# Optimization experiments

Measured on AMD Instinct MI355X. Metric: run time of the kernel, lower is better.

## Reference

```python
import jax, jax.numpy as jnp
import numpy as np

B, F, D, H = 16384, 39, 16, 2   # batch, fields, embed_dim, heads
VOCAB = 10000                    # per-field vocab
DH = D * H                       # attention output dim per layer (no head split)


def setup_inputs() -> dict:
    key = jax.random.key(0)
    ks = jax.random.split(key, 32)
    def n(k, shape, s=0.05):
        return jax.random.normal(k, shape, jnp.float32) * s
    inp = {"x": jax.random.randint(ks[0], (B, F), 0, VOCAB, dtype=jnp.int32)}
    inp["emb"] = n(ks[1], (F * VOCAB, D))
    idx = 2
    for i, din in enumerate([D, DH, DH]):  # layer0: 16->32, layers 1-2: 32->32
        for nm in ["wq", "wk", "wv", "wr"]:
            inp[f"{nm}{i}"] = n(ks[idx], (din, DH)); idx += 1
    prev = F * DH  # 1248 after flatten
    for i, u in enumerate([128, 64, 32, 1], 1):
        inp[f"w{i}"] = n(ks[idx], (prev, u)); idx += 1
        inp[f"b{i}"] = jnp.zeros((u,), jnp.float32)
        prev = u
    return inp


def reference(x, emb,
              wq0, wk0, wv0, wr0,
              wq1, wk1, wv1, wr1,
              wq2, wk2, wv2, wr2,
              w1, b1, w2, b2, w3, b3, w4, b4):
    offsets = jnp.arange(F, dtype=jnp.int32) * VOCAB
    e = emb[x + offsets]                                   # [B, F, D]
    for wq, wk, wv, wr in [(wq0, wk0, wv0, wr0),
                           (wq1, wk1, wv1, wr1),
                           (wq2, wk2, wv2, wr2)]:
        q = jnp.einsum('bfd,de->bfe', e, wq)               # [B, F, DH]
        k = jnp.einsum('bfd,de->bfe', e, wk)
        v = jnp.einsum('bfd,de->bfe', e, wv)
        att = jax.nn.softmax(jnp.einsum('bfe,bge->bfg', q, k), axis=-1)  # [B,F,F], no scaling
        out = jnp.einsum('bfg,bge->bfe', att, v) + jnp.einsum('bfd,de->bfe', e, wr)
        e = jax.nn.relu(out)
    h = e.reshape(B, F * DH)
    for w, b in [(w1, b1), (w2, b2), (w3, b3)]:
        h = jax.nn.relu(h @ w + b)
    return jax.nn.sigmoid(h @ w4 + b4)                     # [B, 1]
```

## Files before the change

### kernel.cpp

```cpp
#include <hip/hip_runtime.h>
#include <math.h>

#define NF   39
#define NB   16384
#define NVOC 10000

typedef unsigned short u16;
typedef unsigned int   u32;
typedef float f32x4 __attribute__((ext_vector_type(4)));
typedef short s16x8 __attribute__((ext_vector_type(8)));

#define E3_U16   20447232u
#define NSWZ     182272

__device__ __forceinline__ u32 bfadj(float x){
    u32 u = __float_as_uint(x);
    return u + 0x7fffu + ((u >> 16) & 1u);
}
__device__ __forceinline__ u32 pk2(float a, float b){
#if __has_builtin(__builtin_amdgcn_cvt_pk_bf16_f32)
    auto t = __builtin_amdgcn_cvt_pk_bf16_f32(a, b);
    u32 r; __builtin_memcpy(&r, &t, 4); return r;
#else
    return __builtin_amdgcn_perm(bfadj(a), bfadj(b), 0x03020706u);
#endif
}
__device__ __forceinline__ u16 f2bf(float f){ return (u16)(bfadj(f) >> 16); }

__device__ __forceinline__ float fexp2(float x){
#if __has_builtin(__builtin_amdgcn_exp2f)
    return __builtin_amdgcn_exp2f(x);
#else
    return exp2f(x);
#endif
}
__device__ __forceinline__ float frcp(float x){
#if __has_builtin(__builtin_amdgcn_rcpf)
    return __builtin_amdgcn_rcpf(x);
#else
    return 1.f / x;
#endif
}

__device__ __forceinline__ void wave_sync(){
    asm volatile("s_waitcnt lgkmcnt(0)" ::: "memory");
}
__device__ __forceinline__ f32x4 mfma16(s16x8 a, s16x8 b, f32x4 c){
    return __builtin_amdgcn_mfma_f32_16x16x32_bf16(a, b, c, 0, 0, 0);
}
__device__ __forceinline__ void store4(u16* p, f32x4 v){
    *(uint2*)p = make_uint2(pk2(v[0], v[1]), pk2(v[2], v[3]));
}

__global__ void __launch_bounds__(256) swz_kernel(
    const float* __restrict__ wq0, const float* __restrict__ wk0,
    const float* __restrict__ wv0, const float* __restrict__ wr0,
    const float* __restrict__ wq1, const float* __restrict__ wk1,
    const float* __restrict__ wv1, const float* __restrict__ wr1,
    const float* __restrict__ wq2, const float* __restrict__ wk2,
    const float* __restrict__ wv2, const float* __restrict__ wr2,
    const float* __restrict__ w1, const float* __restrict__ w2,
    const float* __restrict__ w3, u16* __restrict__ ws)
{
    int gid = (int)blockIdx.x*256 + (int)threadIdx.x;
    if (gid >= NSWZ) return;
    int w    = gid & 511;
    int lane = w >> 3, j = w & 7;
    int n    = lane & 15, quad = lane >> 4;
    int kin  = quad*8 + j;
    float val;
    if (gid < 12288){
        int mat = gid >> 10;
        int nt  = (gid >> 9) & 1;
        const float* W;
        switch (mat){
            case 0: W = wq0; break; case 1: W = wk0; break;
            case 2: W = wv0; break; case 3: W = wr0; break;
            case 4: W = wq1; break; case 5: W = wk1; break;
            case 6: W = wv1; break; case 7: W = wr1; break;
            case 8: W = wq2; break; case 9: W = wk2; break;
            case 10: W = wv2; break; default: W = wr2; break;
        }
        int din = (mat < 4) ? 16 : 32;
        val = (kin < din) ? W[kin*32 + nt*16 + n] : 0.f;
        if ((mat & 3) == 0) val *= 1.44269504f;
    } else if (gid < 12288 + 159744){
        int tt = (gid - 12288) >> 9;
        int ks = tt >> 3, nt = tt & 7;
        val = w1[(ks*32 + kin)*128 + nt*16 + n];
    } else if (gid < 12288 + 159744 + 8192){
        int tt = (gid - (12288+159744)) >> 9;
        int ks = tt >> 2, nt = tt & 3;
        val = w2[(ks*32 + kin)*64 + nt*16 + n];
    } else {
        int tt = (gid - (12288+159744+8192)) >> 9;
        int ks = tt >> 1, nt = tt & 1;
        val = w3[(ks*32 + kin)*32 + nt*16 + n];
    }
    ws[E3_U16 + gid] = f2bf(val);
}

__global__ void __launch_bounds__(256, 4) attn_kernel(
    const int* __restrict__ x, const float* __restrict__ emb,
    u16* __restrict__ ws)
{
    __shared__ __align__(16) u16 lds[4*5120];
    const int tid  = (int)threadIdx.x;
    const int wid  = tid >> 6, lane = tid & 63;
    const int h    = lane >> 4, nl = lane & 15;
    const int r    = (int)blockIdx.x*4 + wid;

    u16* vBuf = lds + wid*5120;
    u16* eBuf = vBuf;
    u16* kBuf = vBuf + 2048;
    u16* qBuf = kBuf + 1536;
    u16* pBuf = kBuf;
    const u16* wmat = ws + E3_U16;
    const f32x4 z = {0.f, 0.f, 0.f, 0.f};
    const int A_off = nl*8 + (h>>1)*128 + (h&1)*4;

    f32x4 ci;
#pragma unroll
    for (int reg = 0; reg < 4; ++reg)
        ci[reg] = (h*4 + reg >= 7) ? -1e30f : 0.f;

    if (lane < 48){
        int f = lane, mt = f >> 4, fl = f & 15;
        u16* row = eBuf + mt*512 + fl*8;
        if (f < NF){
            const float4* ep = (const float4*)(emb + ((size_t)(x[r*NF + f] + f*NVOC))*16);
            float4 e0 = ep[0], e1 = ep[1], e2 = ep[2], e3 = ep[3];
            *(uint4*)(row)       = make_uint4(pk2(e0.x,e0.y), pk2(e0.z,e0.w),
                                              pk2(e1.x,e1.y), pk2(e1.z,e1.w));
            *(uint4*)(row + 128) = make_uint4(pk2(e2.x,e2.y), pk2(e2.z,e2.w),
                                              pk2(e3.x,e3.y), pk2(e3.z,e3.w));
        } else {
            *(uint4*)(row)       = make_uint4(0,0,0,0);
            *(uint4*)(row + 128) = make_uint4(0,0,0,0);
        }
        *(uint4*)(row + 256) = make_uint4(0,0,0,0);
        *(uint4*)(row + 384) = make_uint4(0,0,0,0);
    }
    *(uint2*)(vBuf + 3*512 + 256 + lane*4) = make_uint2(0,0);
    wave_sync();

#pragma unroll 1
    for (int L = 0; L < 3; ++L){
        const u16* wB = wmat + L*4096;
        s16x8 bE[3];
#pragma unroll
        for (int nt = 0; nt < 3; ++nt)
            bE[nt] = *(const s16x8*)(eBuf + nt*512 + lane*8);
        wave_sync();

        {
            s16x8 a0 = *(const s16x8*)(wB + lane*8);
            s16x8 a1 = *(const s16x8*)(wB + 512 + lane*8);
#pragma unroll
            for (int nt = 0; nt < 3; ++nt){
                store4(qBuf + nt*512       + A_off, mfma16(a0, bE[nt], z));
                store4(qBuf + nt*512 + 256 + A_off, mfma16(a1, bE[nt], z));
            }
        }
        {
            s16x8 a0 = *(const s16x8*)(wB + 1024 + lane*8);
            s16x8 a1 = *(const s16x8*)(wB + 1536 + lane*8);
#pragma unroll
            for (int nt = 0; nt < 3; ++nt){
                store4(kBuf + nt*512       + A_off, mfma16(a0, bE[nt], z));
                store4(kBuf + nt*512 + 256 + A_off, mfma16(a1, bE[nt], z));
            }
        }
        {
            s16x8 b0 = *(const s16x8*)(wB + 2048 + lane*8);
            s16x8 b1 = *(const s16x8*)(wB + 2560 + lane*8);
#pragma unroll
            for (int mtg = 0; mtg < 3; ++mtg){
                int toff = (mtg>>1)*1024 + (mtg&1)*256;
                store4(vBuf + toff       + A_off, mfma16(bE[mtg], b0, z));
                store4(vBuf + toff + 512 + A_off, mfma16(bE[mtg], b1, z));
            }
            *(uint2*)(vBuf + 2*512 + 256 + lane*4) = make_uint2(0,0);
        }
        f32x4 R[2][3];
        {
            s16x8 a0 = *(const s16x8*)(wB + 3072 + lane*8);
            s16x8 a1 = *(const s16x8*)(wB + 3584 + lane*8);
#pragma unroll
            for (int nt = 0; nt < 3; ++nt){
                R[0][nt] = mfma16(a0, bE[nt], z);
                R[1][nt] = mfma16(a1, bE[nt], z);
            }
        }
        wave_sync();

        f32x4 S[3][3];
        {
            s16x8 aK[3], bQ[3];
#pragma unroll
            for (int i = 0; i < 3; ++i){
                aK[i] = *(const s16x8*)(kBuf + i*512 + lane*8);
                bQ[i] = *(const s16x8*)(qBuf + i*512 + lane*8);
            }
#pragma unroll
            for (int mtg = 0; mtg < 3; ++mtg)
#pragma unroll
            for (int nt = 0; nt < 3; ++nt)
                S[mtg][nt] = mfma16(aK[mtg], bQ[nt], (mtg == 2) ? ci : z);
        }
        float inv[3];
#pragma unroll
        for (int nt = 0; nt < 3; ++nt){
            float t = 0.f;
#pragma unroll
            for (int mtg = 0; mtg < 3; ++mtg)
#pragma unroll
            for (int reg = 0; reg < 4; ++reg){
                S[mtg][nt][reg] = fexp2(S[mtg][nt][reg]);
                t += S[mtg][nt][reg];
            }
            t += __shfl_xor(t, 16, 64);
            t += __shfl_xor(t, 32, 64);
            inv[nt] = frcp(t);
        }
#pragma unroll
        for (int mtg = 0; mtg < 3; ++mtg)
#pragma unroll
        for (int nt = 0; nt < 3; ++nt)
            store4(pBuf + ((mtg>>1)*3 + nt)*512 + (mtg&1)*256 + A_off, S[mtg][nt]);
        wave_sync();

        s16x8 aV[2][2], bP[2][3];
#pragma unroll
        for (int ks = 0; ks < 2; ++ks){
#pragma unroll
            for (int emt = 0; emt < 2; ++emt)
                aV[ks][emt] = *(const s16x8*)(vBuf + (ks*2+emt)*512 + lane*8);
#pragma unroll
            for (int nt = 0; nt < 3; ++nt)
                bP[ks][nt] = *(const s16x8*)(pBuf + (ks*3+nt)*512 + lane*8);
        }
        wave_sync();
        if (L < 2){
#pragma unroll
            for (int emt = 0; emt < 2; ++emt)
#pragma unroll
            for (int nt = 0; nt < 3; ++nt){
                f32x4 o = mfma16(aV[1][emt], bP[1][nt],
                         mfma16(aV[0][emt], bP[0][nt], z));
                float m = (nt < 2 || nl < 7) ? 1.f : 0.f;
#pragma unroll
                for (int reg = 0; reg < 4; ++reg)
                    o[reg] = fmaxf(fmaf(o[reg], inv[nt], R[emt][nt][reg]), 0.f) * m;
                store4(eBuf + nt*512 + emt*256 + A_off, o);
            }
        } else {
            int st = r >> 4, sm = r & 15;
            u32 base = (u32)(st*39)*512u + (u32)(sm*8 + (h>>1)*128 + (h&1)*4);
#pragma unroll
            for (int emt = 0; emt < 2; ++emt)
#pragma unroll
            for (int nt = 0; nt < 3; ++nt){
                f32x4 o = mfma16(aV[1][emt], bP[1][nt],
                         mfma16(aV[0][emt], bP[0][nt], z));
#pragma unroll
                for (int reg = 0; reg < 4; ++reg)
                    o[reg] = fmaxf(fmaf(o[reg], inv[nt], R[emt][nt][reg]), 0.f);
                int f = nt*16 + nl;
                if (f < NF)
                    *(uint2*)(ws + base + (u32)f*512u + emt*256) =
                        make_uint2(pk2(o[0], o[1]), pk2(o[2], o[3]));
            }
        }
        wave_sync();
    }
}

__global__ void __launch_bounds__(256, 4) mlp_kernel(
    const float* __restrict__ b1, const float* __restrict__ b2,
    const float* __restrict__ b3, const float* __restrict__ w4,
    const float* __restrict__ b4, const u16* __restrict__ ws,
    float* __restrict__ out)
{
    __shared__ __align__(16) float red[8192];
    __shared__ __align__(16) u16 h1t[2048];
    __shared__ __align__(16) u16 h2t[1024];
    __shared__ float part[32];
    const int tid = (int)threadIdx.x;
    const int w   = tid >> 6, lane = tid & 63;
    const int h   = lane >> 4, nl = lane & 15;
    const int st  = (int)blockIdx.x;
    const int A_off = nl*8 + (h>>1)*128 + (h&1)*4;

    const u16* w1b = ws + E3_U16 + 12288u;
    const u16* w2b = w1b + 159744u;
    const u16* w3b = w2b + 8192u;
    const f32x4 z = {0.f,0.f,0.f,0.f};

    f32x4 acc[8];
#pragma unroll
    for (int nt = 0; nt < 8; ++nt) acc[nt] = z;
#pragma unroll 2
    for (int ks = w; ks < 39; ks += 4){
        s16x8 aE = *(const s16x8*)(ws + (u32)(st*39 + ks)*512u + lane*8);
#pragma unroll
        for (int nt = 0; nt < 8; ++nt){
            s16x8 aW = *(const s16x8*)(w1b + (ks*8 + nt)*512 + lane*8);
            acc[nt] = mfma16(aW, aE, acc[nt]);
        }
    }
#pragma unroll
    for (int nt = 0; nt < 8; ++nt)
        *(f32x4*)(red + (w*8 + nt)*256 + lane*4) = acc[nt];
    __syncthreads();

#pragma unroll
    for (int t = 0; t < 2; ++t){
        int ft = 2*w + t;
        f32x4 s = *(const f32x4*)(red + (0*8 + ft)*256 + lane*4);
#pragma unroll
        for (int p = 1; p < 4; ++p){
            f32x4 q = *(const f32x4*)(red + (p*8 + ft)*256 + lane*4);
#pragma unroll
            for (int reg = 0; reg < 4; ++reg) s[reg] += q[reg];
        }
        float4 bv = *(const float4*)(b1 + ft*16 + h*4);
        f32x4 v;
        v[0] = fmaxf(s[0] + bv.x, 0.f);
        v[1] = fmaxf(s[1] + bv.y, 0.f);
        v[2] = fmaxf(s[2] + bv.z, 0.f);
        v[3] = fmaxf(s[3] + bv.w, 0.f);
        store4(h1t + ft*256 + A_off, v);
    }
    __syncthreads();

    {
        f32x4 a2 = z;
#pragma unroll
        for (int ks = 0; ks < 4; ++ks){
            s16x8 aW = *(const s16x8*)(w2b + (ks*4 + w)*512 + lane*8);
            s16x8 bH = *(const s16x8*)(h1t + ks*512 + lane*8);
            a2 = mfma16(aW, bH, a2);
        }
        float4 bv = *(const float4*)(b2 + w*16 + h*4);
        f32x4 v;
        v[0] = fmaxf(a2[0] + bv.x, 0.f);
        v[1] = fmaxf(a2[1] + bv.y, 0.f);
        v[2] = fmaxf(a2[2] + bv.z, 0.f);
        v[3] = fmaxf(a2[3] + bv.w, 0.f);
        store4(h2t + (w>>1)*512 + (w&1)*256 + A_off, v);
    }
    __syncthreads();

    if (w < 2){
        f32x4 a3 = z;
#pragma unroll
        for (int ks = 0; ks < 2; ++ks){
            s16x8 aW = *(const s16x8*)(w3b + (ks*2 + w)*512 + lane*8);
            s16x8 bH = *(const s16x8*)(h2t + ks*512 + lane*8);
            a3 = mfma16(aW, bH, a3);
        }
        float4 b3v = *(const float4*)(b3 + w*16 + h*4);
        float4 w4v = *(const float4*)(w4 + w*16 + h*4);
        float t = fmaxf(a3[0] + b3v.x, 0.f)*w4v.x
                + fmaxf(a3[1] + b3v.y, 0.f)*w4v.y
                + fmaxf(a3[2] + b3v.z, 0.f)*w4v.z
                + fmaxf(a3[3] + b3v.w, 0.f)*w4v.w;
        t += __shfl_xor(t, 16, 64);
        t += __shfl_xor(t, 32, 64);
        if (h == 0) part[w*16 + nl] = t;
    }
    __syncthreads();
    if (tid < 16){
        float zz = part[tid] + part[16 + tid] + b4[0];
        out[st*16 + tid] = 1.f/(1.f + __expf(-zz));
    }
}

extern "C" void kernel_launch(void* const* d_in, const int* in_sizes, int n_in,
                              void* d_out, int out_size, void* d_ws, size_t ws_size,
                              hipStream_t stream)
{
    (void)in_sizes; (void)n_in; (void)ws_size; (void)out_size;
    const int*   x   = (const int*)d_in[0];
    const float* emb = (const float*)d_in[1];
    u16* ws = (u16*)d_ws;

    swz_kernel<<<(NSWZ+255)/256, 256, 0, stream>>>(
        (const float*)d_in[2],  (const float*)d_in[3],  (const float*)d_in[4],  (const float*)d_in[5],
        (const float*)d_in[6],  (const float*)d_in[7],  (const float*)d_in[8],  (const float*)d_in[9],
        (const float*)d_in[10], (const float*)d_in[11], (const float*)d_in[12], (const float*)d_in[13],
        (const float*)d_in[14], (const float*)d_in[16], (const float*)d_in[18], ws);

    attn_kernel<<<NB/4, 256, 0, stream>>>(x, emb, ws);

    mlp_kernel<<<NB/16, 256, 0, stream>>>(
        (const float*)d_in[15], (const float*)d_in[17], (const float*)d_in[19],
        (const float*)d_in[20], (const float*)d_in[21], ws, (float*)d_out);
}
```

Before: 186.8 us.

## Fold Wq·Wkᵀ into one matrix and keep attention fragments in registers via permlane swaps

The weight-prep kernel now precomputes G = Wq·Wkᵀ (scaled by log2 e) per layer, so attention scores become E·G·Eᵀ and the separate Q and K projections go away. The attention kernel no longer round-trips Q, K, V, P and the layer output through LDS. It converts MFMA accumulator layouts into operand fragments in registers using v_permlane16/32_swap, and reduces the softmax row sums the same way. This cuts LDS traffic, the waitcnt syncs, and the per-wave LDS footprint, at the cost of extra permute instructions and a serial 32-term dot product per element in the prep kernel.

```diff
diff --git a/kernel.cpp b/kernel.cpp
--- a/kernel.cpp
+++ b/kernel.cpp
@@ -11,7 +11,8 @@
 typedef short s16x8 __attribute__((ext_vector_type(8)));
 
 #define E3_U16   20447232u
-#define NSWZ     182272
+#define WOFF_W1  9216u
+#define NSWZ     179200
 
 __device__ __forceinline__ u32 bfadj(float x){
     u32 u = __float_as_uint(x);
@@ -50,6 +51,32 @@
 }
 __device__ __forceinline__ void store4(u16* p, f32x4 v){
     *(uint2*)p = make_uint2(pk2(v[0], v[1]), pk2(v[2], v[3]));
+}
+
+__device__ __forceinline__ void swap32(u32 &a, u32 &b){
+    asm("v_permlane32_swap_b32 %0, %1" : "+v"(a), "+v"(b));
+}
+__device__ __forceinline__ void swap16(u32 &a, u32 &b){
+    asm("v_permlane16_swap_b32 %0, %1" : "+v"(a), "+v"(b));
+}
+__device__ __forceinline__ s16x8 fragCC(f32x4 A, f32x4 B){
+    u32 a0 = pk2(A[0], A[1]), b0 = pk2(B[0], B[1]);
+    u32 a1 = pk2(A[2], A[3]), b1 = pk2(B[2], B[3]);
+    swap32(a0, b0); swap16(a0, b0);
+    swap32(a1, b1); swap16(a1, b1);
+    union { u32 w[4]; s16x8 v; } u;
+    u.w[0] = a0; u.w[1] = a1; u.w[2] = b0; u.w[3] = b1;
+    return u.v;
+}
+__device__ __forceinline__ float xadd16(float t){
+    u32 a = __float_as_uint(t), b = a;
+    swap16(a, b);
+    return __uint_as_float(a) + __uint_as_float(b);
+}
+__device__ __forceinline__ float xadd32(float t){
+    u32 a = __float_as_uint(t), b = a;
+    swap32(a, b);
+    return __uint_as_float(a) + __uint_as_float(b);
 }
 
 __global__ void __launch_bounds__(256) swz_kernel(
@@ -69,31 +96,40 @@
     int n    = lane & 15, quad = lane >> 4;
     int kin  = quad*8 + j;
     float val;
-    if (gid < 12288){
-        int mat = gid >> 10;
-        int nt  = (gid >> 9) & 1;
-        const float* W;
-        switch (mat){
-            case 0: W = wq0; break; case 1: W = wk0; break;
-            case 2: W = wv0; break; case 3: W = wr0; break;
-            case 4: W = wq1; break; case 5: W = wk1; break;
-            case 6: W = wv1; break; case 7: W = wr1; break;
-            case 8: W = wq2; break; case 9: W = wk2; break;
-            case 10: W = wv2; break; default: W = wr2; break;
-        }
-        int din = (mat < 4) ? 16 : 32;
-        val = (kin < din) ? W[kin*32 + nt*16 + n] : 0.f;
-        if ((mat & 3) == 0) val *= 1.44269504f;
-    } else if (gid < 12288 + 159744){
-        int tt = (gid - 12288) >> 9;
+    if (gid < 9216){
+        int l = gid / 3072;
+        int rr = gid - l*3072;
+        int kind = rr >> 10;
+        int a    = (rr >> 9) & 1;
+        int din  = l ? 32 : 16;
+        const float *WQ, *WK, *WV, *WR;
+        if (l == 0){ WQ=wq0; WK=wk0; WV=wv0; WR=wr0; }
+        else if (l == 1){ WQ=wq1; WK=wk1; WV=wv1; WR=wr1; }
+        else { WQ=wq2; WK=wk2; WV=wv2; WR=wr2; }
+        if (kind == 0){
+            int dp = a*16 + n;
+            float s = 0.f;
+            if (dp < din && kin < din){
+                float acc = 0.f;
+                for (int e = 0; e < 32; ++e)
+                    acc += WQ[kin*32 + e] * WK[dp*32 + e];
+                s = acc * 1.44269504f;
+            }
+            val = s;
+        } else {
+            const float* W = (kind == 1) ? WV : WR;
+            val = (kin < din) ? W[kin*32 + a*16 + n] : 0.f;
+        }
+    } else if (gid < 9216 + 159744){
+        int tt = (gid - 9216) >> 9;
         int ks = tt >> 3, nt = tt & 7;
         val = w1[(ks*32 + kin)*128 + nt*16 + n];
-    } else if (gid < 12288 + 159744 + 8192){
-        int tt = (gid - (12288+159744)) >> 9;
+    } else if (gid < 9216 + 159744 + 8192){
+        int tt = (gid - (9216+159744)) >> 9;
         int ks = tt >> 2, nt = tt & 3;
         val = w2[(ks*32 + kin)*64 + nt*16 + n];
     } else {
-        int tt = (gid - (12288+159744+8192)) >> 9;
+        int tt = (gid - (9216+159744+8192)) >> 9;
         int ks = tt >> 1, nt = tt & 1;
         val = w3[(ks*32 + kin)*32 + nt*16 + n];
     }
@@ -104,20 +140,15 @@
     const int* __restrict__ x, const float* __restrict__ emb,
     u16* __restrict__ ws)
 {
-    __shared__ __align__(16) u16 lds[4*5120];
+    __shared__ __align__(16) u16 lds[4*1536];
     const int tid  = (int)threadIdx.x;
     const int wid  = tid >> 6, lane = tid & 63;
     const int h    = lane >> 4, nl = lane & 15;
     const int r    = (int)blockIdx.x*4 + wid;
 
-    u16* vBuf = lds + wid*5120;
-    u16* eBuf = vBuf;
-    u16* kBuf = vBuf + 2048;
-    u16* qBuf = kBuf + 1536;
-    u16* pBuf = kBuf;
+    u16* eBuf = lds + wid*1536;
     const u16* wmat = ws + E3_U16;
     const f32x4 z = {0.f, 0.f, 0.f, 0.f};
-    const int A_off = nl*8 + (h>>1)*128 + (h&1)*4;
 
     f32x4 ci;
 #pragma unroll
@@ -141,73 +172,45 @@
         *(uint4*)(row + 256) = make_uint4(0,0,0,0);
         *(uint4*)(row + 384) = make_uint4(0,0,0,0);
     }
-    *(uint2*)(vBuf + 3*512 + 256 + lane*4) = make_uint2(0,0);
     wave_sync();
+    s16x8 bE[3];
+#pragma unroll
+    for (int nt = 0; nt < 3; ++nt)
+        bE[nt] = *(const s16x8*)(eBuf + nt*512 + lane*8);
 
 #pragma unroll 1
     for (int L = 0; L < 3; ++L){
-        const u16* wB = wmat + L*4096;
-        s16x8 bE[3];
+        const u16* wL = wmat + L*3072;
+
+        s16x8 bT[3];
+        {
+            s16x8 g0 = *(const s16x8*)(wL +       lane*8);
+            s16x8 g1 = *(const s16x8*)(wL + 512 + lane*8);
+#pragma unroll
+            for (int nt = 0; nt < 3; ++nt)
+                bT[nt] = fragCC(mfma16(g0, bE[nt], z), mfma16(g1, bE[nt], z));
+        }
+        s16x8 aV[2][2];
+        {
+            s16x8 v0 = *(const s16x8*)(wL + 1024 + lane*8);
+            s16x8 v1 = *(const s16x8*)(wL + 1536 + lane*8);
+#pragma unroll
+            for (int emt = 0; emt < 2; ++emt){
+                s16x8 vb = emt ? v1 : v0;
+                f32x4 c0 = mfma16(bE[0], vb, z);
+                f32x4 c1 = mfma16(bE[1], vb, z);
+                f32x4 c2 = mfma16(bE[2], vb, z);
+                aV[0][emt] = fragCC(c0, c1);
+                aV[1][emt] = fragCC(c2, z);
+            }
+        }
+        f32x4 S[3][3];
+#pragma unroll
+        for (int mtg = 0; mtg < 3; ++mtg)
 #pragma unroll
         for (int nt = 0; nt < 3; ++nt)
-            bE[nt] = *(const s16x8*)(eBuf + nt*512 + lane*8);
-        wave_sync();
-
-        {
-            s16x8 a0 = *(const s16x8*)(wB + lane*8);
-            s16x8 a1 = *(const s16x8*)(wB + 512 + lane*8);
-#pragma unroll
-            for (int nt = 0; nt < 3; ++nt){
-                store4(qBuf + nt*512       + A_off, mfma16(a0, bE[nt], z));
-                store4(qBuf + nt*512 + 256 + A_off, mfma16(a1, bE[nt], z));
-            }
-        }
-        {
-            s16x8 a0 = *(const s16x8*)(wB + 1024 + lane*8);
-            s16x8 a1 = *(const s16x8*)(wB + 1536 + lane*8);
-#pragma unroll
-            for (int nt = 0; nt < 3; ++nt){
-                store4(kBuf + nt*512       + A_off, mfma16(a0, bE[nt], z));
-                store4(kBuf + nt*512 + 256 + A_off, mfma16(a1, bE[nt], z));
-            }
-        }
-        {
-            s16x8 b0 = *(const s16x8*)(wB + 2048 + lane*8);
-            s16x8 b1 = *(const s16x8*)(wB + 2560 + lane*8);
-#pragma unroll
-            for (int mtg = 0; mtg < 3; ++mtg){
-                int toff = (mtg>>1)*1024 + (mtg&1)*256;
-                store4(vBuf + toff       + A_off, mfma16(bE[mtg], b0, z));
-                store4(vBuf + toff + 512 + A_off, mfma16(bE[mtg], b1, z));
-            }
-            *(uint2*)(vBuf + 2*512 + 256 + lane*4) = make_uint2(0,0);
-        }
-        f32x4 R[2][3];
-        {
-            s16x8 a0 = *(const s16x8*)(wB + 3072 + lane*8);
-            s16x8 a1 = *(const s16x8*)(wB + 3584 + lane*8);
-#pragma unroll
-            for (int nt = 0; nt < 3; ++nt){
-                R[0][nt] = mfma16(a0, bE[nt], z);
-                R[1][nt] = mfma16(a1, bE[nt], z);
-            }
-        }
-        wave_sync();
-
-        f32x4 S[3][3];
-        {
-            s16x8 aK[3], bQ[3];
-#pragma unroll
-            for (int i = 0; i < 3; ++i){
-                aK[i] = *(const s16x8*)(kBuf + i*512 + lane*8);
-                bQ[i] = *(const s16x8*)(qBuf + i*512 + lane*8);
-            }
-#pragma unroll
-            for (int mtg = 0; mtg < 3; ++mtg)
-#pragma unroll
-            for (int nt = 0; nt < 3; ++nt)
-                S[mtg][nt] = mfma16(aK[mtg], bQ[nt], (mtg == 2) ? ci : z);
-        }
+            S[mtg][nt] = mfma16(bE[mtg], bT[nt], (mtg == 2) ? ci : z);
+
         float inv[3];
 #pragma unroll
         for (int nt = 0; nt < 3; ++nt){
@@ -219,60 +222,55 @@
                 S[mtg][nt][reg] = fexp2(S[mtg][nt][reg]);
                 t += S[mtg][nt][reg];
             }
-            t += __shfl_xor(t, 16, 64);
-            t += __shfl_xor(t, 32, 64);
-            inv[nt] = frcp(t);
-        }
-#pragma unroll
-        for (int mtg = 0; mtg < 3; ++mtg)
-#pragma unroll
-        for (int nt = 0; nt < 3; ++nt)
-            store4(pBuf + ((mtg>>1)*3 + nt)*512 + (mtg&1)*256 + A_off, S[mtg][nt]);
-        wave_sync();
-
-        s16x8 aV[2][2], bP[2][3];
-#pragma unroll
-        for (int ks = 0; ks < 2; ++ks){
-#pragma unroll
-            for (int emt = 0; emt < 2; ++emt)
-                aV[ks][emt] = *(const s16x8*)(vBuf + (ks*2+emt)*512 + lane*8);
-#pragma unroll
-            for (int nt = 0; nt < 3; ++nt)
-                bP[ks][nt] = *(const s16x8*)(pBuf + (ks*3+nt)*512 + lane*8);
-        }
-        wave_sync();
+            inv[nt] = frcp(xadd32(xadd16(t)));
+        }
+        f32x4 R[2][3];
+        {
+            s16x8 r0 = *(const s16x8*)(wL + 2048 + lane*8);
+            s16x8 r1 = *(const s16x8*)(wL + 2560 + lane*8);
+#pragma unroll
+            for (int nt = 0; nt < 3; ++nt){
+                R[0][nt] = mfma16(r0, bE[nt], z);
+                R[1][nt] = mfma16(r1, bE[nt], z);
+            }
+        }
         if (L < 2){
 #pragma unroll
-            for (int emt = 0; emt < 2; ++emt)
-#pragma unroll
             for (int nt = 0; nt < 3; ++nt){
-                f32x4 o = mfma16(aV[1][emt], bP[1][nt],
-                         mfma16(aV[0][emt], bP[0][nt], z));
+                s16x8 p0 = fragCC(S[0][nt], S[1][nt]);
+                s16x8 p1 = fragCC(S[2][nt], z);
                 float m = (nt < 2 || nl < 7) ? 1.f : 0.f;
-#pragma unroll
-                for (int reg = 0; reg < 4; ++reg)
-                    o[reg] = fmaxf(fmaf(o[reg], inv[nt], R[emt][nt][reg]), 0.f) * m;
-                store4(eBuf + nt*512 + emt*256 + A_off, o);
+                f32x4 oc[2];
+#pragma unroll
+                for (int emt = 0; emt < 2; ++emt){
+                    f32x4 o = mfma16(aV[1][emt], p1, mfma16(aV[0][emt], p0, z));
+#pragma unroll
+                    for (int reg = 0; reg < 4; ++reg)
+                        o[reg] = fmaxf(fmaf(o[reg], inv[nt], R[emt][nt][reg]), 0.f) * m;
+                    oc[emt] = o;
+                }
+                bE[nt] = fragCC(oc[0], oc[1]);
             }
         } else {
             int st = r >> 4, sm = r & 15;
             u32 base = (u32)(st*39)*512u + (u32)(sm*8 + (h>>1)*128 + (h&1)*4);
 #pragma unroll
-            for (int emt = 0; emt < 2; ++emt)
-#pragma unroll
             for (int nt = 0; nt < 3; ++nt){
-                f32x4 o = mfma16(aV[1][emt], bP[1][nt],
-                         mfma16(aV[0][emt], bP[0][nt], z));
-#pragma unroll
-                for (int reg = 0; reg < 4; ++reg)
-                    o[reg] = fmaxf(fmaf(o[reg], inv[nt], R[emt][nt][reg]), 0.f);
+                s16x8 p0 = fragCC(S[0][nt], S[1][nt]);
+                s16x8 p1 = fragCC(S[2][nt], z);
                 int f = nt*16 + nl;
-                if (f < NF)
-                    *(uint2*)(ws + base + (u32)f*512u + emt*256) =
-                        make_uint2(pk2(o[0], o[1]), pk2(o[2], o[3]));
-            }
-        }
-        wave_sync();
+#pragma unroll
+                for (int emt = 0; emt < 2; ++emt){
+                    f32x4 o = mfma16(aV[1][emt], p1, mfma16(aV[0][emt], p0, z));
+#pragma unroll
+                    for (int reg = 0; reg < 4; ++reg)
+                        o[reg] = fmaxf(fmaf(o[reg], inv[nt], R[emt][nt][reg]), 0.f);
+                    if (f < NF)
+                        *(uint2*)(ws + base + (u32)f*512u + emt*256) =
+                            make_uint2(pk2(o[0], o[1]), pk2(o[2], o[3]));
+                }
+            }
+        }
     }
 }
 
@@ -292,7 +290,7 @@
     const int st  = (int)blockIdx.x;
     const int A_off = nl*8 + (h>>1)*128 + (h&1)*4;
 
-    const u16* w1b = ws + E3_U16 + 12288u;
+    const u16* w1b = ws + E3_U16 + WOFF_W1;
     const u16* w2b = w1b + 159744u;
     const u16* w3b = w2b + 8192u;
     const f32x4 z = {0.f,0.f,0.f,0.f};
```

Result: no change. 189.2 us (+1.2%).
